# Kernel optimization log

Hardware: AMD Instinct MI355X
Metric: run time of the kernel (lower is better)

The kernel has to match this reference:

```python
import jax, jax.numpy as jnp
import numpy as np

H = 32        # num attention heads
KVH = 8       # num key/value heads
G = H // KVH  # kv groups
D = 128       # head dim
LATENT = 256
ROPE_BASE = 10000.0
LN_EPS = 1e-5


def setup_inputs() -> dict:
    key = jax.random.key(0)
    ks = jax.random.split(key, 8)
    B, S, H2 = 2, 1024, 8192
    s = 0.02  # weight init scale
    return {
        "hidden_states": jax.random.normal(ks[0], (B, S, H2), jnp.float32),
        "position_ids": jnp.sort(jax.random.randint(ks[1], (B, S), 0, S), axis=-1),
        "Wq": jax.random.normal(ks[2], (H * D, H2), jnp.float32) * s,
        "Wdkv": jax.random.normal(ks[3], (LATENT, H2), jnp.float32) * s,
        "ln_gamma": jnp.ones((LATENT,), jnp.float32),
        "ln_beta": jnp.zeros((LATENT,), jnp.float32),
        "Wuk": jax.random.normal(ks[4], (KVH * D, LATENT), jnp.float32) * s,
        "Wuv": jax.random.normal(ks[5], (KVH * D, LATENT), jnp.float32) * s,
        "Wo": jax.random.normal(ks[6], (H * D, H * D), jnp.float32) * s,
    }


def _rope_tables(seq_len, dim, dtype):
    inv_freq = 1.0 / (ROPE_BASE ** (jnp.arange(0, dim, 2, dtype=jnp.float32) / dim))
    t = jnp.arange(seq_len, dtype=jnp.float32)
    freqs = t[:, None] * inv_freq[None, :]          # [S, dim/2]
    emb = jnp.concatenate([freqs, freqs], axis=-1)  # [S, dim]
    return jnp.cos(emb).astype(dtype), jnp.sin(emb).astype(dtype)


def _rotate_half(x):
    x1, x2 = jnp.split(x, 2, axis=-1)
    return jnp.concatenate([-x2, x1], axis=-1)


def _apply_rope(x, cos, sin, position_ids):
    # x: [B, h, S, D]; cos/sin: [S_cache, D]; position_ids: [B, S]
    c = cos[position_ids][:, None]  # [B, 1, S, D]
    s = sin[position_ids][:, None]
    return x * c + _rotate_half(x) * s


def _layer_norm(x, gamma, beta):
    mu = jnp.mean(x, axis=-1, keepdims=True)
    var = jnp.mean(jnp.square(x - mu), axis=-1, keepdims=True)
    return (x - mu) * jax.lax.rsqrt(var + LN_EPS) * gamma + beta


def reference(hidden_states, position_ids, Wq, Wdkv, ln_gamma, ln_beta, Wuk, Wuv, Wo):
    B, S, _ = hidden_states.shape
    dtype = hidden_states.dtype

    # Q projection -> [B, H, S, D]
    q = (hidden_states @ Wq.T).reshape(B, S, H, D).transpose(0, 2, 1, 3)

    # MLA compress + norm: [B, S, LATENT]
    c_kv = _layer_norm(hidden_states @ Wdkv.T, ln_gamma, ln_beta)

    # RoPE on full head_dim (rope_dim == 0 path)
    cos, sin = _rope_tables(S, D, dtype)
    q = _apply_rope(q, cos, sin, position_ids)

    # Decompress K/V -> [B, KVH, S, D]
    k = (c_kv @ Wuk.T).reshape(B, S, KVH, D).transpose(0, 2, 1, 3)
    v = (c_kv @ Wuv.T).reshape(B, S, KVH, D).transpose(0, 2, 1, 3)
    k = _apply_rope(k, cos, sin, position_ids)

    # Grouped-query attention (repeat_kv expressed via group axis), causal
    qg = q.reshape(B, KVH, G, S, D)
    scale = 1.0 / jnp.sqrt(jnp.asarray(D, dtype))
    scores = jnp.einsum('bhgqd,bhkd->bhgqk', qg, k) * scale  # [B,KVH,G,S,S]
    causal = jnp.arange(S)[:, None] >= jnp.arange(S)[None, :]
    scores = jnp.where(causal, scores, jnp.asarray(-jnp.inf, dtype))
    probs = jax.nn.softmax(scores, axis=-1)
    attn = jnp.einsum('bhgqk,bhkd->bhgqd', probs, v)          # [B,KVH,G,S,D]
    attn = attn.reshape(B, H, S, D).transpose(0, 2, 1, 3).reshape(B, S, H * D)

    return attn @ Wo.T  # [B, S, hidden_size]
```

## Files before the change

### kernel.cpp

```cpp
#include <hip/hip_runtime.h>
#include <hip/hip_bf16.h>

using f32x4 = __attribute__((ext_vector_type(4))) float;
using s16x8 = __attribute__((ext_vector_type(8))) short;

__device__ __forceinline__ ushort f2b(float f) {
  union { float f; unsigned u; } v; v.f = f;
  unsigned r = v.u + 0x7fff + ((v.u >> 16) & 1);
  return (ushort)(r >> 16);
}
__device__ __forceinline__ float b2f(ushort u) {
  union { unsigned u; float f; } v; v.u = ((unsigned)u) << 16;
  return v.f;
}

__device__ __forceinline__ void load_lds16(const ushort* g, ushort* l) {
  __builtin_amdgcn_global_load_lds((const __attribute__((address_space(1))) unsigned int*)g,
                                   (__attribute__((address_space(3))) unsigned int*)l,
                                   16, 0, 0);
}

__device__ __forceinline__ void cast_seg(const float* __restrict__ in, ushort* __restrict__ out,
                                         int n8, int tid, int stride) {
  const float4* i4 = (const float4*)in;
  for (int i = tid; i < n8; i += stride) {
    float4 a = i4[i * 2];
    float4 b = i4[i * 2 + 1];
    s16x8 o;
    o[0] = f2b(a.x); o[1] = f2b(a.y); o[2] = f2b(a.z); o[3] = f2b(a.w);
    o[4] = f2b(b.x); o[5] = f2b(b.y); o[6] = f2b(b.z); o[7] = f2b(b.w);
    *(s16x8*)(out + (size_t)i * 8) = o;
  }
}

__global__ void cast6_kernel(const float* a0, ushort* b0, int n0,
                             const float* a1, ushort* b1, int n1,
                             const float* a2, ushort* b2, int n2,
                             const float* a3, ushort* b3, int n3,
                             const float* a4, ushort* b4, int n4,
                             const float* a5, ushort* b5, int n5) {
  int tid = blockIdx.x * blockDim.x + threadIdx.x;
  int stride = gridDim.x * blockDim.x;
  cast_seg(a0, b0, n0, tid, stride);
  cast_seg(a1, b1, n1, tid, stride);
  cast_seg(a2, b2, n2, tid, stride);
  cast_seg(a3, b3, n3, tid, stride);
  cast_seg(a4, b4, n4, tid, stride);
  cast_seg(a5, b5, n5, tid, stride);
}

__global__ void rope_table_kernel(const int* __restrict__ pos,
                                  float* __restrict__ cosb, float* __restrict__ sinb) {
  int i = blockIdx.x * 256 + threadIdx.x;
  int d = i & 63;
  float invf = exp2f(-(float)d * (13.287712379549449f / 64.0f));
  float ang = (float)pos[i >> 6] * invf;
  cosb[i] = cosf(ang);
  sinb[i] = sinf(ang);
}

__global__ void ln_kernel(const float* __restrict__ X, const float* __restrict__ gamma,
                          const float* __restrict__ beta, ushort* __restrict__ out) {
  int row = blockIdx.x * 4 + (threadIdx.x >> 6);
  int lane = threadIdx.x & 63;
  float4 x = {0.f, 0.f, 0.f, 0.f};
#pragma unroll
  for (int sp = 0; sp < 8; ++sp) {
    const float4 t = *(const float4*)(X + (size_t)sp * 2048 * 256 + (size_t)row * 256 + lane * 4);
    x.x += t.x; x.y += t.y; x.z += t.z; x.w += t.w;
  }
  float s = x.x + x.y + x.z + x.w;
  for (int m = 32; m >= 1; m >>= 1) s += __shfl_xor(s, m);
  float mu = s * (1.0f / 256.0f);
  float dx = x.x - mu, dy = x.y - mu, dz = x.z - mu, dw = x.w - mu;
  float v = dx * dx + dy * dy + dz * dz + dw * dw;
  for (int m = 32; m >= 1; m >>= 1) v += __shfl_xor(v, m);
  float inv = rsqrtf(v * (1.0f / 256.0f) + 1e-5f);
  const float4 g = *(const float4*)(gamma + lane * 4);
  const float4 bt = *(const float4*)(beta + lane * 4);
  ushort4 o;
  o.x = f2b(dx * inv * g.x + bt.x);
  o.y = f2b(dy * inv * g.y + bt.y);
  o.z = f2b(dz * inv * g.z + bt.z);
  o.w = f2b(dw * inv * g.w + bt.w);
  *(ushort4*)(out + (size_t)row * 256 + lane * 4) = o;
}

template<int NH>
__global__ void rope_apply_bf16(ushort* __restrict__ X, const float* __restrict__ cosb,
                                const float* __restrict__ sinb) {
  int bs = blockIdx.x;
  ushort* xr = X + (size_t)bs * (NH * 128);
  int p = threadIdx.x;
  if (p < NH * 8) {
    int h = p >> 3, c8 = p & 7;
    int idx = h * 128 + c8 * 8;
    s16x8 x1 = *(s16x8*)(xr + idx);
    s16x8 x2 = *(s16x8*)(xr + idx + 64);
    const float* cb = cosb + (bs << 6) + c8 * 8;
    const float* sb = sinb + (bs << 6) + c8 * 8;
    s16x8 o1, o2;
#pragma unroll
    for (int j = 0; j < 8; ++j) {
      float a = b2f((ushort)x1[j]), bb = b2f((ushort)x2[j]);
      float c = cb[j], s = sb[j];
      o1[j] = f2b(a * c - bb * s);
      o2[j] = f2b(bb * c + a * s);
    }
    *(s16x8*)(xr + idx) = o1;
    *(s16x8*)(xr + idx + 64) = o2;
  }
}

__global__ void qred_rope_kernel(const float* __restrict__ P, const float* __restrict__ cosb,
                                 const float* __restrict__ sinb, ushort* __restrict__ out) {
  int bs = blockIdx.x;
  int p = threadIdx.x;
  int h = p >> 3, c8 = p & 7;
  size_t base = (size_t)bs * 4096 + h * 128 + c8 * 8;
  const float* p0 = P + base;
  const float* p1 = P + 2048ull * 4096 + base;
  float4 a0 = *(const float4*)(p0);
  float4 a1 = *(const float4*)(p0 + 4);
  float4 b0 = *(const float4*)(p1);
  float4 b1 = *(const float4*)(p1 + 4);
  float4 c0 = *(const float4*)(p0 + 64);
  float4 c1 = *(const float4*)(p0 + 68);
  float4 d0 = *(const float4*)(p1 + 64);
  float4 d1 = *(const float4*)(p1 + 68);
  float x1[8] = {a0.x + b0.x, a0.y + b0.y, a0.z + b0.z, a0.w + b0.w,
                 a1.x + b1.x, a1.y + b1.y, a1.z + b1.z, a1.w + b1.w};
  float x2[8] = {c0.x + d0.x, c0.y + d0.y, c0.z + d0.z, c0.w + d0.w,
                 c1.x + d1.x, c1.y + d1.y, c1.z + d1.z, c1.w + d1.w};
  const float* cb = cosb + (bs << 6) + c8 * 8;
  const float* sb = sinb + (bs << 6) + c8 * 8;
  s16x8 o1, o2;
#pragma unroll
  for (int j = 0; j < 8; ++j) {
    float c = cb[j], s = sb[j];
    o1[j] = f2b(x1[j] * c - x2[j] * s);
    o2[j] = f2b(x2[j] * c + x1[j] * s);
  }
  ushort* orow = out + base;
  *(s16x8*)(orow) = o1;
  *(s16x8*)(orow + 64) = o2;
}

__global__ void ored_kernel(const float* __restrict__ P, float* __restrict__ out, int n4) {
  int stride = gridDim.x * blockDim.x;
  const float4* q0 = (const float4*)P;
  const float4* q1 = (const float4*)(P + 2048ull * 4096);
  for (int i = blockIdx.x * blockDim.x + threadIdx.x; i < n4; i += stride) {
    float4 a = q0[i], b = q1[i];
    float4 o = {a.x + b.x, a.y + b.y, a.z + b.z, a.w + b.w};
    ((float4*)out)[i] = o;
  }
}

__global__ __launch_bounds__(256, 2)
void gemm2_bt(const ushort* __restrict__ A, int lda, const ushort* __restrict__ B, int ldb,
              float* __restrict__ C, int M, int N, int Kloop) {
  __shared__ ushort lA[3][128 * 32];
  __shared__ ushort lB[3][256 * 32];
  const int gx = gridDim.x;
  const int nwg = gx * gridDim.y;
  const int bid = blockIdx.y * gx + blockIdx.x;
  const int cpx = nwg >> 3;
  const int swz = (bid & 7) * cpx + (bid >> 3);
  const int bm = (swz / gx) * 128;
  const int bn = (swz % gx) * 256;
  const int lane = threadIdx.x & 63;
  const int w = threadIdx.x >> 6;
  const int wm = w >> 1, wn = w & 1;
  const int l15 = lane & 15, l4 = lane >> 4;
  const int lr = lane >> 2;
  const int lc = lane & 3;

  f32x4 acc[4][8] = {};

  const ushort* Abase = A + (size_t)blockIdx.z * Kloop;
  const ushort* Bbase = B + (size_t)blockIdx.z * Kloop;

  auto stage = [&](int bb, int k0) {
#pragma unroll
    for (int p = 0; p < 2; ++p) {
      int row0 = w * 32 + p * 16;
      int r = row0 + lr;
      const ushort* src = Abase + (size_t)(bm + r) * lda + k0 + (lc ^ (r & 3)) * 8;
      load_lds16(src, &lA[bb][row0 * 32]);
    }
#pragma unroll
    for (int p = 0; p < 4; ++p) {
      int row0 = w * 64 + p * 16;
      int r = row0 + lr;
      const ushort* src = Bbase + (size_t)(bn + r) * ldb + k0 + (lc ^ (r & 3)) * 8;
      load_lds16(src, &lB[bb][row0 * 32]);
    }
  };

  const int nt = Kloop / 32;
  stage(0, 0);
  stage(1, 32);
  asm volatile("s_waitcnt vmcnt(6)" ::: "memory");
  __builtin_amdgcn_s_barrier();

  int cur = 0;
  for (int t = 0; t < nt; ++t) {
    if (t + 2 < nt) stage(cur == 0 ? 2 : cur - 1, (t + 2) * 32);
    __builtin_amdgcn_sched_barrier(0);
    s16x8 bf[8], af[4];
#pragma unroll
    for (int g = 0; g < 8; ++g) {
      int r = wn * 128 + g * 16 + l15;
      bf[g] = *(const s16x8*)&lB[cur][r * 32 + (l4 ^ (r & 3)) * 8];
    }
#pragma unroll
    for (int f = 0; f < 4; ++f) {
      int r = wm * 64 + f * 16 + l15;
      af[f] = *(const s16x8*)&lA[cur][r * 32 + (l4 ^ (r & 3)) * 8];
    }
    __builtin_amdgcn_s_setprio(1);
#pragma unroll
    for (int f = 0; f < 4; ++f)
#pragma unroll
      for (int g = 0; g < 8; ++g)
        acc[f][g] = __builtin_amdgcn_mfma_f32_16x16x32_bf16(af[f], bf[g], acc[f][g], 0, 0, 0);
    __builtin_amdgcn_s_setprio(0);
    __builtin_amdgcn_sched_barrier(0);
    if (t + 1 < nt) {
      if (t + 2 < nt) asm volatile("s_waitcnt vmcnt(6)" ::: "memory");
      else            asm volatile("s_waitcnt vmcnt(0)" ::: "memory");
      __builtin_amdgcn_s_barrier();
    }
    cur = (cur == 2) ? 0 : cur + 1;
  }

  const size_t cz = (size_t)blockIdx.z * M * N;
#pragma unroll
  for (int f = 0; f < 4; ++f)
#pragma unroll
    for (int g = 0; g < 8; ++g)
#pragma unroll
      for (int rr = 0; rr < 4; ++rr) {
        int row = bm + wm * 64 + f * 16 + l4 * 4 + rr;
        int col = bn + wn * 128 + g * 16 + l15;
        C[cz + (size_t)row * N + col] = acc[f][g][rr];
      }
}

template<bool BF16_OUT>
__global__ __launch_bounds__(256, 2)
void gemm_bt(const ushort* __restrict__ A, int lda, const ushort* __restrict__ B, int ldb,
             void* __restrict__ Cv, int M, int N, int Kloop) {
  __shared__ ushort lA[128 * 64];
  __shared__ ushort lB[128 * 64];
  const int nwg = gridDim.x * gridDim.y;
  const int bid = blockIdx.y * gridDim.x + blockIdx.x;
  const int cpx = nwg >> 3;
  const int swz = (bid & 7) * cpx + (bid >> 3);
  const int bm = (swz / gridDim.x) * 128;
  const int bn = (swz % gridDim.x) * 128;
  const int t = threadIdx.x;
  const int lane = t & 63;
  const int w = t >> 6;
  const int wr = (w >> 1) * 64, wc = (w & 1) * 64;
  const int l15 = lane & 15, l4 = lane >> 4;

  f32x4 acc[4][4] = {};

  const ushort* Ag = A + (size_t)blockIdx.z * Kloop +
                     (size_t)(bm + w * 8 + (lane >> 3)) * lda + (lane & 7) * 8;
  const ushort* Bg = B + (size_t)blockIdx.z * Kloop +
                     (size_t)(bn + w * 8 + (lane >> 3)) * ldb + (lane & 7) * 8;
  ushort* lAw = lA + w * 8 * 64;
  ushort* lBw = lB + w * 8 * 64;

  for (int k0 = 0; k0 < Kloop; k0 += 64) {
    __syncthreads();
#pragma unroll
    for (int p = 0; p < 4; ++p) {
      load_lds16(Ag + (size_t)(p * 32) * lda + k0, lAw + p * 32 * 64);
      load_lds16(Bg + (size_t)(p * 32) * ldb + k0, lBw + p * 32 * 64);
    }
    __syncthreads();
#pragma unroll
    for (int kk = 0; kk < 2; ++kk) {
      s16x8 af[4], bf[4];
#pragma unroll
      for (int i = 0; i < 4; ++i)
        af[i] = *(const s16x8*)(lA + (wr + i * 16 + l15) * 64 + kk * 32 + l4 * 8);
#pragma unroll
      for (int j = 0; j < 4; ++j)
        bf[j] = *(const s16x8*)(lB + (wc + j * 16 + l15) * 64 + kk * 32 + l4 * 8);
#pragma unroll
      for (int i = 0; i < 4; ++i)
#pragma unroll
        for (int j = 0; j < 4; ++j)
          acc[i][j] = __builtin_amdgcn_mfma_f32_16x16x32_bf16(af[i], bf[j], acc[i][j], 0, 0, 0);
    }
  }

  const size_t cz = (size_t)blockIdx.z * M * N;
#pragma unroll
  for (int i = 0; i < 4; ++i)
#pragma unroll
    for (int j = 0; j < 4; ++j)
#pragma unroll
      for (int r = 0; r < 4; ++r) {
        int row = bm + wr + i * 16 + l4 * 4 + r;
        int col = bn + wc + j * 16 + l15;
        if (BF16_OUT)
          ((ushort*)Cv)[cz + (size_t)row * N + col] = f2b(acc[i][j][r]);
        else
          ((float*)Cv)[cz + (size_t)row * N + col] = acc[i][j][r];
      }
}

__global__ __launch_bounds__(256, 2)
void attn_kernel(const ushort* __restrict__ Q, const ushort* __restrict__ Kb,
                 const ushort* __restrict__ Vt, ushort* __restrict__ O) {
  __shared__ ushort Kl[2][64 * 128];
  __shared__ ushort Vl[2][128 * 64];
  __shared__ ushort Plds[4][16][64];
  const int bx = blockIdx.x;
  const int qb = bx & 15;
  const int h = (bx >> 4) & 31;
  const int b = bx >> 9;
  const int kvh = h >> 2;
  const int w = threadIdx.x >> 6;
  const int lane = threadIdx.x & 63;
  const int l15 = lane & 15, l4 = lane >> 4;

  const int q0 = qb * 64 + w * 16;

  s16x8 aq[4];
  const ushort* qrow = Q + (size_t)(b * 1024 + q0 + l15) * 4096 + h * 128 + l4 * 8;
#pragma unroll
  for (int kk = 0; kk < 4; ++kk) aq[kk] = *(const s16x8*)(qrow + kk * 32);

  auto stageK = [&](int bb, int t) {
#pragma unroll
    for (int i = 0; i < 4; ++i) {
      int row = w * 16 + i * 4 + (lane >> 4);
      int cg = (lane & 15) ^ (row & 7);
      const ushort* src = Kb + (size_t)(b * 1024 + t * 64 + row) * 1024 + kvh * 128 + cg * 8;
      load_lds16(src, &Kl[bb][(w * 16 + i * 4) * 128]);
    }
  };
  auto stageV = [&](int bb, int t) {
#pragma unroll
    for (int i = 0; i < 4; ++i) {
      int d = w * 32 + i * 8 + (lane >> 3);
      int cg = (lane & 7) ^ (d & 7);
      const ushort* src = Vt + (size_t)(kvh * 128 + d) * 2048 + b * 1024 + t * 64 + cg * 8;
      load_lds16(src, &Vl[bb][(w * 32 + i * 8) * 64]);
    }
  };

  f32x4 o_acc[8] = {};
  float M_[4] = {-1e30f, -1e30f, -1e30f, -1e30f};
  float L_[4] = {0.f, 0.f, 0.f, 0.f};

  const int nt = qb + 1;
  int buf = 0;
  stageK(0, 0);
  stageV(0, 0);
  __syncthreads();

  for (int t = 0; t < nt; ++t) {
    if (t + 1 < nt) {
      stageK(buf ^ 1, t + 1);
      stageV(buf ^ 1, t + 1);
    }

    f32x4 s_acc[4] = {};
#pragma unroll
    for (int ns = 0; ns < 4; ++ns) {
      int r = ns * 16 + l15;
#pragma unroll
      for (int kk = 0; kk < 4; ++kk) {
        s16x8 kf = *(const s16x8*)&Kl[buf][r * 128 + (((kk * 4 + l4) ^ (r & 7)) * 8)];
        s_acc[ns] = __builtin_amdgcn_mfma_f32_16x16x32_bf16(aq[kk], kf, s_acc[ns], 0, 0, 0);
      }
    }

    float p[4][4];
    const bool diag = (t == qb);
#pragma unroll
    for (int ns = 0; ns < 4; ++ns)
#pragma unroll
      for (int r = 0; r < 4; ++r) {
        float s = s_acc[ns][r] * 0.08838834764831845f;
        if (diag) {
          int kvi = t * 64 + ns * 16 + l15;
          int qi = q0 + l4 * 4 + r;
          if (kvi > qi) s = -1e30f;
        }
        p[ns][r] = s;
      }

#pragma unroll
    for (int r = 0; r < 4; ++r) {
      float mt = fmaxf(fmaxf(p[0][r], p[1][r]), fmaxf(p[2][r], p[3][r]));
      mt = fmaxf(mt, __shfl_xor(mt, 1));
      mt = fmaxf(mt, __shfl_xor(mt, 2));
      mt = fmaxf(mt, __shfl_xor(mt, 4));
      mt = fmaxf(mt, __shfl_xor(mt, 8));
      float nm = fmaxf(M_[r], mt);
      float sf = __expf(M_[r] - nm);
      M_[r] = nm;
      float ls = 0.f;
#pragma unroll
      for (int ns = 0; ns < 4; ++ns) {
        float e = __expf(p[ns][r] - nm);
        p[ns][r] = e;
        ls += e;
      }
      ls += __shfl_xor(ls, 1);
      ls += __shfl_xor(ls, 2);
      ls += __shfl_xor(ls, 4);
      ls += __shfl_xor(ls, 8);
      L_[r] = L_[r] * sf + ls;
#pragma unroll
      for (int ds_ = 0; ds_ < 8; ++ds_) o_acc[ds_][r] *= sf;
    }

#pragma unroll
    for (int ns = 0; ns < 4; ++ns)
#pragma unroll
      for (int r = 0; r < 4; ++r)
        Plds[w][l4 * 4 + r][ns * 16 + l15] = f2b(p[ns][r]);
    asm volatile("s_waitcnt lgkmcnt(0)" ::: "memory");
    __builtin_amdgcn_sched_barrier(0);
    s16x8 pf[2];
    pf[0] = *(const s16x8*)&Plds[w][l15][l4 * 8];
    pf[1] = *(const s16x8*)&Plds[w][l15][32 + l4 * 8];

#pragma unroll
    for (int ds_ = 0; ds_ < 8; ++ds_) {
      int d = ds_ * 16 + l15;
#pragma unroll
      for (int kk2 = 0; kk2 < 2; ++kk2) {
        s16x8 vf = *(const s16x8*)&Vl[buf][d * 64 + (((kk2 * 4 + l4) ^ (d & 7)) * 8)];
        o_acc[ds_] = __builtin_amdgcn_mfma_f32_16x16x32_bf16(pf[kk2], vf, o_acc[ds_], 0, 0, 0);
      }
    }

    __syncthreads();
    buf ^= 1;
  }

#pragma unroll
  for (int r = 0; r < 4; ++r) {
    float invl = 1.0f / L_[r];
#pragma unroll
    for (int ds_ = 0; ds_ < 8; ++ds_)
      O[(size_t)(b * 1024 + q0 + l4 * 4 + r) * 4096 + h * 128 + ds_ * 16 + l15] =
          f2b(o_acc[ds_][r] * invl);
  }
}

extern "C" void kernel_launch(void* const* d_in, const int* in_sizes, int n_in,
                              void* d_out, int out_size, void* d_ws, size_t ws_size,
                              hipStream_t stream) {
  const float* hs = (const float*)d_in[0];
  const int* pos = (const int*)d_in[1];
  const float* Wq = (const float*)d_in[2];
  const float* Wdkv = (const float*)d_in[3];
  const float* gam = (const float*)d_in[4];
  const float* bet = (const float*)d_in[5];
  const float* Wuk = (const float*)d_in[6];
  const float* Wuv = (const float*)d_in[7];
  const float* Wo = (const float*)d_in[8];
  float* out = (float*)d_out;

  char* ws = (char*)d_ws;
  size_t off = 0;
  auto alloc = [&](size_t bytes) {
    char* p = ws + off;
    off += (bytes + 255) & ~(size_t)255;
    return p;
  };
  ushort* hs_b = (ushort*)alloc(2048ull * 8192 * 2);
  ushort* Wq_b = (ushort*)alloc(4096ull * 8192 * 2);
  ushort* Wdkv_b = (ushort*)alloc(256ull * 8192 * 2);
  ushort* Wuk_b = (ushort*)alloc(1024ull * 256 * 2);
  ushort* Wuv_b = (ushort*)alloc(1024ull * 256 * 2);
  ushort* Wo_b = (ushort*)alloc(4096ull * 4096 * 2);
  float* cosb = (float*)alloc(2048ull * 64 * 4);
  float* sinb = (float*)alloc(2048ull * 64 * 4);
  float* ckv_part = (float*)alloc(8ull * 2048 * 256 * 4);
  ushort* ckv_b = (ushort*)alloc(2048ull * 256 * 2);
  float* qo_part = (float*)alloc(2ull * 2048 * 4096 * 4);
  ushort* q_b = (ushort*)alloc(2048ull * 4096 * 2);
  ushort* k_b = (ushort*)alloc(2048ull * 1024 * 2);
  ushort* vt_b = (ushort*)alloc(1024ull * 2048 * 2);
  ushort* at_b = (ushort*)alloc(2048ull * 4096 * 2);
  (void)ws_size; (void)in_sizes; (void)n_in; (void)out_size;

  cast6_kernel<<<2048, 256, 0, stream>>>(
      hs, hs_b, (int)(2048ull * 8192 / 8),
      Wq, Wq_b, (int)(4096ull * 8192 / 8),
      Wdkv, Wdkv_b, (int)(256ull * 8192 / 8),
      Wuk, Wuk_b, (int)(1024ull * 256 / 8),
      Wuv, Wuv_b, (int)(1024ull * 256 / 8),
      Wo, Wo_b, (int)(4096ull * 4096 / 8));

  rope_table_kernel<<<512, 256, 0, stream>>>(pos, cosb, sinb);

  gemm_bt<false><<<dim3(2, 16, 8), 256, 0, stream>>>(hs_b, 8192, Wdkv_b, 8192,
                                                     ckv_part, 2048, 256, 1024);
  ln_kernel<<<512, 256, 0, stream>>>(ckv_part, gam, bet, ckv_b);

  gemm2_bt<<<dim3(16, 16, 2), 256, 0, stream>>>(hs_b, 8192, Wq_b, 8192,
                                                qo_part, 2048, 4096, 4096);
  qred_rope_kernel<<<2048, 256, 0, stream>>>(qo_part, cosb, sinb, q_b);

  gemm_bt<true><<<dim3(8, 16), 256, 0, stream>>>(ckv_b, 256, Wuk_b, 256,
                                                 k_b, 2048, 1024, 256);
  rope_apply_bf16<8><<<2048, 256, 0, stream>>>(k_b, cosb, sinb);

  gemm_bt<true><<<dim3(16, 8), 256, 0, stream>>>(Wuv_b, 256, ckv_b, 256,
                                                 vt_b, 1024, 2048, 256);

  attn_kernel<<<1024, 256, 0, stream>>>(q_b, k_b, vt_b, at_b);

  gemm2_bt<<<dim3(16, 16, 2), 256, 0, stream>>>(at_b, 4096, Wo_b, 4096,
                                                qo_part, 2048, 4096, 2048);
  ored_kernel<<<2048, 256, 0, stream>>>(qo_part, out, (int)(2048ull * 4096 / 4));
}
```

Baseline: 509.9 us.

## Replace split-K GEMM with 256x256-tile 8-wave kernel using ping-pong LDS phases

Replaces the 128x256-tile, 4-wave, triple-buffered GEMM used for the Q and output projections with a 256x256-tile, 8-wave kernel. It uses a K-step of 64, double buffering, and a four-phase schedule that interleaves LDS fragment reads with MFMA bursts, separated by barriers and priority changes. The larger tile raises arithmetic intensity per byte loaded and halves the number of workgroups. The cost is 128KB of LDS per block, which likely limits occupancy to one block per CU. It also adds many barriers per iteration and waits for all loads (vmcnt(0)) at the end of each step, which weakens load prefetching.

New measurement: 530.9 us. 4.1% more time.

```diff
diff --git a/kernel.cpp b/kernel.cpp
--- a/kernel.cpp
+++ b/kernel.cpp
@@ -3,6 +3,8 @@
 
 using f32x4 = __attribute__((ext_vector_type(4))) float;
 using s16x8 = __attribute__((ext_vector_type(8))) short;
+
+#define MFMA __builtin_amdgcn_mfma_f32_16x16x32_bf16
 
 __device__ __forceinline__ ushort f2b(float f) {
   union { float f; unsigned u; } v; v.f = f;
@@ -157,93 +159,132 @@
   }
 }
 
-__global__ __launch_bounds__(256, 2)
-void gemm2_bt(const ushort* __restrict__ A, int lda, const ushort* __restrict__ B, int ldb,
+__global__ __launch_bounds__(512, 2)
+void gemm8_bt(const ushort* __restrict__ A, int lda, const ushort* __restrict__ B, int ldb,
               float* __restrict__ C, int M, int N, int Kloop) {
-  __shared__ ushort lA[3][128 * 32];
-  __shared__ ushort lB[3][256 * 32];
+  __shared__ ushort lA[2][256 * 64];
+  __shared__ ushort lB[2][256 * 64];
   const int gx = gridDim.x;
   const int nwg = gx * gridDim.y;
   const int bid = blockIdx.y * gx + blockIdx.x;
   const int cpx = nwg >> 3;
   const int swz = (bid & 7) * cpx + (bid >> 3);
-  const int bm = (swz / gx) * 128;
+  const int bm = (swz / gx) * 256;
   const int bn = (swz % gx) * 256;
-  const int lane = threadIdx.x & 63;
-  const int w = threadIdx.x >> 6;
-  const int wm = w >> 1, wn = w & 1;
+  const int tid = threadIdx.x;
+  const int lane = tid & 63;
+  const int w = tid >> 6;
+  const int wm = w >> 2, wn = w & 3;
   const int l15 = lane & 15, l4 = lane >> 4;
-  const int lr = lane >> 2;
-  const int lc = lane & 3;
-
-  f32x4 acc[4][8] = {};
+
+  f32x4 acc[8][4] = {};
 
   const ushort* Abase = A + (size_t)blockIdx.z * Kloop;
   const ushort* Bbase = B + (size_t)blockIdx.z * Kloop;
+  const int srow = tid >> 3;
+  const int sswz = (tid & 7) ^ (srow & 7);
 
   auto stage = [&](int bb, int k0) {
-#pragma unroll
-    for (int p = 0; p < 2; ++p) {
-      int row0 = w * 32 + p * 16;
-      int r = row0 + lr;
-      const ushort* src = Abase + (size_t)(bm + r) * lda + k0 + (lc ^ (r & 3)) * 8;
-      load_lds16(src, &lA[bb][row0 * 32]);
-    }
-#pragma unroll
-    for (int p = 0; p < 4; ++p) {
-      int row0 = w * 64 + p * 16;
-      int r = row0 + lr;
-      const ushort* src = Bbase + (size_t)(bn + r) * ldb + k0 + (lc ^ (r & 3)) * 8;
-      load_lds16(src, &lB[bb][row0 * 32]);
-    }
+    const int rl = w * 8;
+#pragma unroll
+    for (int h = 0; h < 2; ++h)
+#pragma unroll
+      for (int p = 0; p < 2; ++p) {
+        int row = h * 128 + p * 64 + srow;
+        load_lds16(Abase + (size_t)(bm + row) * lda + k0 + sswz * 8,
+                   &lA[bb][(h * 128 + p * 64 + rl) * 64]);
+        load_lds16(Bbase + (size_t)(bn + row) * ldb + k0 + sswz * 8,
+                   &lB[bb][(h * 128 + p * 64 + rl) * 64]);
+      }
   };
-
-  const int nt = Kloop / 32;
+  auto rdA = [&](int bb, int f, int kk) -> s16x8 {
+    int r = wm * 128 + f * 16 + l15;
+    return *(const s16x8*)&lA[bb][r * 64 + ((kk * 4 + l4) ^ (l15 & 7)) * 8];
+  };
+  auto rdB = [&](int bb, int g, int kk) -> s16x8 {
+    int r = wn * 64 + g * 16 + l15;
+    return *(const s16x8*)&lB[bb][r * 64 + ((kk * 4 + l4) ^ (l15 & 7)) * 8];
+  };
+
+  const int nt = Kloop / 64;
   stage(0, 0);
-  stage(1, 32);
-  asm volatile("s_waitcnt vmcnt(6)" ::: "memory");
+  asm volatile("s_waitcnt vmcnt(0)" ::: "memory");
   __builtin_amdgcn_s_barrier();
 
-  int cur = 0;
+  s16x8 a[8], b[8];
   for (int t = 0; t < nt; ++t) {
-    if (t + 2 < nt) stage(cur == 0 ? 2 : cur - 1, (t + 2) * 32);
+    const int cur = t & 1;
+    if (t + 1 < nt) stage(cur ^ 1, (t + 1) * 64);
     __builtin_amdgcn_sched_barrier(0);
-    s16x8 bf[8], af[4];
-#pragma unroll
-    for (int g = 0; g < 8; ++g) {
-      int r = wn * 128 + g * 16 + l15;
-      bf[g] = *(const s16x8*)&lB[cur][r * 32 + (l4 ^ (r & 3)) * 8];
-    }
-#pragma unroll
-    for (int f = 0; f < 4; ++f) {
-      int r = wm * 64 + f * 16 + l15;
-      af[f] = *(const s16x8*)&lA[cur][r * 32 + (l4 ^ (r & 3)) * 8];
-    }
+#pragma unroll
+    for (int f = 0; f < 4; ++f) { a[2 * f] = rdA(cur, f, 0); a[2 * f + 1] = rdA(cur, f, 1); }
+    b[0] = rdB(cur, 0, 0); b[1] = rdB(cur, 0, 1);
+    b[2] = rdB(cur, 1, 0); b[3] = rdB(cur, 1, 1);
+    __builtin_amdgcn_s_barrier();
+    asm volatile("s_waitcnt lgkmcnt(0)" ::: "memory");
+    __builtin_amdgcn_sched_barrier(0);
     __builtin_amdgcn_s_setprio(1);
 #pragma unroll
     for (int f = 0; f < 4; ++f)
 #pragma unroll
-      for (int g = 0; g < 8; ++g)
-        acc[f][g] = __builtin_amdgcn_mfma_f32_16x16x32_bf16(af[f], bf[g], acc[f][g], 0, 0, 0);
+      for (int g = 0; g < 2; ++g) {
+        acc[f][g] = MFMA(a[2 * f], b[g * 2], acc[f][g], 0, 0, 0);
+        acc[f][g] = MFMA(a[2 * f + 1], b[g * 2 + 1], acc[f][g], 0, 0, 0);
+      }
     __builtin_amdgcn_s_setprio(0);
+    __builtin_amdgcn_s_barrier();
+    b[4] = rdB(cur, 2, 0); b[5] = rdB(cur, 2, 1);
+    b[6] = rdB(cur, 3, 0); b[7] = rdB(cur, 3, 1);
+    __builtin_amdgcn_s_barrier();
+    asm volatile("s_waitcnt lgkmcnt(0)" ::: "memory");
     __builtin_amdgcn_sched_barrier(0);
-    if (t + 1 < nt) {
-      if (t + 2 < nt) asm volatile("s_waitcnt vmcnt(6)" ::: "memory");
-      else            asm volatile("s_waitcnt vmcnt(0)" ::: "memory");
-      __builtin_amdgcn_s_barrier();
-    }
-    cur = (cur == 2) ? 0 : cur + 1;
+    __builtin_amdgcn_s_setprio(1);
+#pragma unroll
+    for (int f = 0; f < 4; ++f)
+#pragma unroll
+      for (int g = 2; g < 4; ++g) {
+        acc[f][g] = MFMA(a[2 * f], b[g * 2], acc[f][g], 0, 0, 0);
+        acc[f][g] = MFMA(a[2 * f + 1], b[g * 2 + 1], acc[f][g], 0, 0, 0);
+      }
+    __builtin_amdgcn_s_setprio(0);
+    __builtin_amdgcn_s_barrier();
+#pragma unroll
+    for (int f = 0; f < 4; ++f) { a[2 * f] = rdA(cur, 4 + f, 0); a[2 * f + 1] = rdA(cur, 4 + f, 1); }
+    __builtin_amdgcn_s_barrier();
+    asm volatile("s_waitcnt lgkmcnt(0)" ::: "memory");
+    __builtin_amdgcn_sched_barrier(0);
+    __builtin_amdgcn_s_setprio(1);
+#pragma unroll
+    for (int f = 0; f < 4; ++f)
+#pragma unroll
+      for (int g = 2; g < 4; ++g) {
+        acc[4 + f][g] = MFMA(a[2 * f], b[g * 2], acc[4 + f][g], 0, 0, 0);
+        acc[4 + f][g] = MFMA(a[2 * f + 1], b[g * 2 + 1], acc[4 + f][g], 0, 0, 0);
+      }
+    __builtin_amdgcn_s_setprio(0);
+    __builtin_amdgcn_s_barrier();
+    __builtin_amdgcn_s_setprio(1);
+#pragma unroll
+    for (int f = 0; f < 4; ++f)
+#pragma unroll
+      for (int g = 0; g < 2; ++g) {
+        acc[4 + f][g] = MFMA(a[2 * f], b[g * 2], acc[4 + f][g], 0, 0, 0);
+        acc[4 + f][g] = MFMA(a[2 * f + 1], b[g * 2 + 1], acc[4 + f][g], 0, 0, 0);
+      }
+    __builtin_amdgcn_s_setprio(0);
+    if (t + 1 < nt) asm volatile("s_waitcnt vmcnt(0)" ::: "memory");
+    __builtin_amdgcn_s_barrier();
   }
 
   const size_t cz = (size_t)blockIdx.z * M * N;
 #pragma unroll
-  for (int f = 0; f < 4; ++f)
-#pragma unroll
-    for (int g = 0; g < 8; ++g)
+  for (int f = 0; f < 8; ++f)
+#pragma unroll
+    for (int g = 0; g < 4; ++g)
 #pragma unroll
       for (int rr = 0; rr < 4; ++rr) {
-        int row = bm + wm * 64 + f * 16 + l4 * 4 + rr;
-        int col = bn + wn * 128 + g * 16 + l15;
+        int row = bm + wm * 128 + f * 16 + l4 * 4 + rr;
+        int col = bn + wn * 64 + g * 16 + l15;
         C[cz + (size_t)row * N + col] = acc[f][g][rr];
       }
 }
@@ -296,7 +337,7 @@
       for (int i = 0; i < 4; ++i)
 #pragma unroll
         for (int j = 0; j < 4; ++j)
-          acc[i][j] = __builtin_amdgcn_mfma_f32_16x16x32_bf16(af[i], bf[j], acc[i][j], 0, 0, 0);
+          acc[i][j] = MFMA(af[i], bf[j], acc[i][j], 0, 0, 0);
     }
   }
 
@@ -380,7 +421,7 @@
 #pragma unroll
       for (int kk = 0; kk < 4; ++kk) {
         s16x8 kf = *(const s16x8*)&Kl[buf][r * 128 + (((kk * 4 + l4) ^ (r & 7)) * 8)];
-        s_acc[ns] = __builtin_amdgcn_mfma_f32_16x16x32_bf16(aq[kk], kf, s_acc[ns], 0, 0, 0);
+        s_acc[ns] = MFMA(aq[kk], kf, s_acc[ns], 0, 0, 0);
       }
     }
 
@@ -442,7 +483,7 @@
 #pragma unroll
       for (int kk2 = 0; kk2 < 2; ++kk2) {
         s16x8 vf = *(const s16x8*)&Vl[buf][d * 64 + (((kk2 * 4 + l4) ^ (d & 7)) * 8)];
-        o_acc[ds_] = __builtin_amdgcn_mfma_f32_16x16x32_bf16(pf[kk2], vf, o_acc[ds_], 0, 0, 0);
+        o_acc[ds_] = MFMA(pf[kk2], vf, o_acc[ds_], 0, 0, 0);
       }
     }
 
@@ -512,8 +553,8 @@
                                                      ckv_part, 2048, 256, 1024);
   ln_kernel<<<512, 256, 0, stream>>>(ckv_part, gam, bet, ckv_b);
 
-  gemm2_bt<<<dim3(16, 16, 2), 256, 0, stream>>>(hs_b, 8192, Wq_b, 8192,
-                                                qo_part, 2048, 4096, 4096);
+  gemm8_bt<<<dim3(16, 8, 2), 512, 0, stream>>>(hs_b, 8192, Wq_b, 8192,
+                                               qo_part, 2048, 4096, 4096);
   qred_rope_kernel<<<2048, 256, 0, stream>>>(qo_part, cosb, sinb, q_b);
 
   gemm_bt<true><<<dim3(8, 16), 256, 0, stream>>>(ckv_b, 256, Wuk_b, 256,
@@ -525,7 +566,7 @@
 
   attn_kernel<<<1024, 256, 0, stream>>>(q_b, k_b, vt_b, at_b);
 
-  gemm2_bt<<<dim3(16, 16, 2), 256, 0, stream>>>(at_b, 4096, Wo_b, 4096,
-                                                qo_part, 2048, 4096, 2048);
+  gemm8_bt<<<dim3(16, 8, 2), 512, 0, stream>>>(at_b, 4096, Wo_b, 4096,
+                                               qo_part, 2048, 4096, 2048);
   ored_kernel<<<2048, 256, 0, stream>>>(qo_part, out, (int)(2048ull * 4096 / 4));
 }
```

## Enlarge attention query tile to 128 rows and store Q split-K partials as bf16

Applied to the files above, without the earlier changes.

The attention kernel now runs 512 threads (8 waves) over 128-query tiles, so each staged K/V tile is reused by twice as many query rows and the number of blocks is halved. Batch 1 walks its query blocks in reverse, and the diagonal mask check becomes per-wave. The Q projection GEMM now writes its two split-K partials as bf16 instead of fp32, and the reduce+RoPE kernel reads bf16, halving that traffic. The cost is some extra rounding error in the Q partial sums, plus wasted masked work for waves whose queries sit below the diagonal K tiles.

Measured after the change: 467.4 us. 1.09x faster.

```diff
diff --git a/kernel.cpp b/kernel.cpp
--- a/kernel.cpp
+++ b/kernel.cpp
@@ -3,6 +3,8 @@
 
 using f32x4 = __attribute__((ext_vector_type(4))) float;
 using s16x8 = __attribute__((ext_vector_type(8))) short;
+
+#define MFMA __builtin_amdgcn_mfma_f32_16x16x32_bf16
 
 __device__ __forceinline__ ushort f2b(float f) {
   union { float f; unsigned u; } v; v.f = f;
@@ -112,34 +114,26 @@
   }
 }
 
-__global__ void qred_rope_kernel(const float* __restrict__ P, const float* __restrict__ cosb,
+__global__ void qred_rope_kernel(const ushort* __restrict__ P, const float* __restrict__ cosb,
                                  const float* __restrict__ sinb, ushort* __restrict__ out) {
   int bs = blockIdx.x;
   int p = threadIdx.x;
   int h = p >> 3, c8 = p & 7;
   size_t base = (size_t)bs * 4096 + h * 128 + c8 * 8;
-  const float* p0 = P + base;
-  const float* p1 = P + 2048ull * 4096 + base;
-  float4 a0 = *(const float4*)(p0);
-  float4 a1 = *(const float4*)(p0 + 4);
-  float4 b0 = *(const float4*)(p1);
-  float4 b1 = *(const float4*)(p1 + 4);
-  float4 c0 = *(const float4*)(p0 + 64);
-  float4 c1 = *(const float4*)(p0 + 68);
-  float4 d0 = *(const float4*)(p1 + 64);
-  float4 d1 = *(const float4*)(p1 + 68);
-  float x1[8] = {a0.x + b0.x, a0.y + b0.y, a0.z + b0.z, a0.w + b0.w,
-                 a1.x + b1.x, a1.y + b1.y, a1.z + b1.z, a1.w + b1.w};
-  float x2[8] = {c0.x + d0.x, c0.y + d0.y, c0.z + d0.z, c0.w + d0.w,
-                 c1.x + d1.x, c1.y + d1.y, c1.z + d1.z, c1.w + d1.w};
+  s16x8 a0 = *(const s16x8*)(P + base);
+  s16x8 b0 = *(const s16x8*)(P + 2048ull * 4096 + base);
+  s16x8 c0 = *(const s16x8*)(P + base + 64);
+  s16x8 d0 = *(const s16x8*)(P + 2048ull * 4096 + base + 64);
   const float* cb = cosb + (bs << 6) + c8 * 8;
   const float* sb = sinb + (bs << 6) + c8 * 8;
   s16x8 o1, o2;
 #pragma unroll
   for (int j = 0; j < 8; ++j) {
+    float x1 = b2f((ushort)a0[j]) + b2f((ushort)b0[j]);
+    float x2 = b2f((ushort)c0[j]) + b2f((ushort)d0[j]);
     float c = cb[j], s = sb[j];
-    o1[j] = f2b(x1[j] * c - x2[j] * s);
-    o2[j] = f2b(x2[j] * c + x1[j] * s);
+    o1[j] = f2b(x1 * c - x2 * s);
+    o2[j] = f2b(x2 * c + x1 * s);
   }
   ushort* orow = out + base;
   *(s16x8*)(orow) = o1;
@@ -157,9 +151,10 @@
   }
 }
 
+template<bool BF16_OUT>
 __global__ __launch_bounds__(256, 2)
 void gemm2_bt(const ushort* __restrict__ A, int lda, const ushort* __restrict__ B, int ldb,
-              float* __restrict__ C, int M, int N, int Kloop) {
+              void* __restrict__ Cv, int M, int N, int Kloop) {
   __shared__ ushort lA[3][128 * 32];
   __shared__ ushort lB[3][256 * 32];
   const int gx = gridDim.x;
@@ -224,7 +219,7 @@
     for (int f = 0; f < 4; ++f)
 #pragma unroll
       for (int g = 0; g < 8; ++g)
-        acc[f][g] = __builtin_amdgcn_mfma_f32_16x16x32_bf16(af[f], bf[g], acc[f][g], 0, 0, 0);
+        acc[f][g] = MFMA(af[f], bf[g], acc[f][g], 0, 0, 0);
     __builtin_amdgcn_s_setprio(0);
     __builtin_amdgcn_sched_barrier(0);
     if (t + 1 < nt) {
@@ -244,7 +239,10 @@
       for (int rr = 0; rr < 4; ++rr) {
         int row = bm + wm * 64 + f * 16 + l4 * 4 + rr;
         int col = bn + wn * 128 + g * 16 + l15;
-        C[cz + (size_t)row * N + col] = acc[f][g][rr];
+        if (BF16_OUT)
+          ((ushort*)Cv)[cz + (size_t)row * N + col] = f2b(acc[f][g][rr]);
+        else
+          ((float*)Cv)[cz + (size_t)row * N + col] = acc[f][g][rr];
       }
 }
 
@@ -296,7 +294,7 @@
       for (int i = 0; i < 4; ++i)
 #pragma unroll
         for (int j = 0; j < 4; ++j)
-          acc[i][j] = __builtin_amdgcn_mfma_f32_16x16x32_bf16(af[i], bf[j], acc[i][j], 0, 0, 0);
+          acc[i][j] = MFMA(af[i], bf[j], acc[i][j], 0, 0, 0);
     }
   }
 
@@ -316,22 +314,22 @@
       }
 }
 
-__global__ __launch_bounds__(256, 2)
+__global__ __launch_bounds__(512, 2)
 void attn_kernel(const ushort* __restrict__ Q, const ushort* __restrict__ Kb,
                  const ushort* __restrict__ Vt, ushort* __restrict__ O) {
   __shared__ ushort Kl[2][64 * 128];
   __shared__ ushort Vl[2][128 * 64];
-  __shared__ ushort Plds[4][16][64];
+  __shared__ ushort Plds[8][16][64];
   const int bx = blockIdx.x;
-  const int qb = bx & 15;
-  const int h = (bx >> 4) & 31;
-  const int b = bx >> 9;
+  const int b = bx >> 8;
+  const int qb = b ? (7 - (bx & 7)) : (bx & 7);
+  const int h = (bx >> 3) & 31;
   const int kvh = h >> 2;
   const int w = threadIdx.x >> 6;
   const int lane = threadIdx.x & 63;
   const int l15 = lane & 15, l4 = lane >> 4;
 
-  const int q0 = qb * 64 + w * 16;
+  const int q0 = qb * 128 + w * 16;
 
   s16x8 aq[4];
   const ushort* qrow = Q + (size_t)(b * 1024 + q0 + l15) * 4096 + h * 128 + l4 * 8;
@@ -340,20 +338,22 @@
 
   auto stageK = [&](int bb, int t) {
 #pragma unroll
-    for (int i = 0; i < 4; ++i) {
-      int row = w * 16 + i * 4 + (lane >> 4);
+    for (int i = 0; i < 2; ++i) {
+      int row0 = w * 8 + i * 4;
+      int row = row0 + (lane >> 4);
       int cg = (lane & 15) ^ (row & 7);
       const ushort* src = Kb + (size_t)(b * 1024 + t * 64 + row) * 1024 + kvh * 128 + cg * 8;
-      load_lds16(src, &Kl[bb][(w * 16 + i * 4) * 128]);
+      load_lds16(src, &Kl[bb][row0 * 128]);
     }
   };
   auto stageV = [&](int bb, int t) {
 #pragma unroll
-    for (int i = 0; i < 4; ++i) {
-      int d = w * 32 + i * 8 + (lane >> 3);
+    for (int i = 0; i < 2; ++i) {
+      int d0 = w * 16 + i * 8;
+      int d = d0 + (lane >> 3);
       int cg = (lane & 7) ^ (d & 7);
       const ushort* src = Vt + (size_t)(kvh * 128 + d) * 2048 + b * 1024 + t * 64 + cg * 8;
-      load_lds16(src, &Vl[bb][(w * 32 + i * 8) * 64]);
+      load_lds16(src, &Vl[bb][d0 * 64]);
     }
   };
 
@@ -361,7 +361,7 @@
   float M_[4] = {-1e30f, -1e30f, -1e30f, -1e30f};
   float L_[4] = {0.f, 0.f, 0.f, 0.f};
 
-  const int nt = qb + 1;
+  const int nt = 2 * qb + 2;
   int buf = 0;
   stageK(0, 0);
   stageV(0, 0);
@@ -380,12 +380,12 @@
 #pragma unroll
       for (int kk = 0; kk < 4; ++kk) {
         s16x8 kf = *(const s16x8*)&Kl[buf][r * 128 + (((kk * 4 + l4) ^ (r & 7)) * 8)];
-        s_acc[ns] = __builtin_amdgcn_mfma_f32_16x16x32_bf16(aq[kk], kf, s_acc[ns], 0, 0, 0);
+        s_acc[ns] = MFMA(aq[kk], kf, s_acc[ns], 0, 0, 0);
       }
     }
 
     float p[4][4];
-    const bool diag = (t == qb);
+    const bool diag = (t * 64 + 63 > q0);
 #pragma unroll
     for (int ns = 0; ns < 4; ++ns)
 #pragma unroll
@@ -442,7 +442,7 @@
 #pragma unroll
       for (int kk2 = 0; kk2 < 2; ++kk2) {
         s16x8 vf = *(const s16x8*)&Vl[buf][d * 64 + (((kk2 * 4 + l4) ^ (d & 7)) * 8)];
-        o_acc[ds_] = __builtin_amdgcn_mfma_f32_16x16x32_bf16(pf[kk2], vf, o_acc[ds_], 0, 0, 0);
+        o_acc[ds_] = MFMA(pf[kk2], vf, o_acc[ds_], 0, 0, 0);
       }
     }
 
@@ -492,6 +492,7 @@
   float* ckv_part = (float*)alloc(8ull * 2048 * 256 * 4);
   ushort* ckv_b = (ushort*)alloc(2048ull * 256 * 2);
   float* qo_part = (float*)alloc(2ull * 2048 * 4096 * 4);
+  ushort* qp_b = (ushort*)alloc(2ull * 2048 * 4096 * 2);
   ushort* q_b = (ushort*)alloc(2048ull * 4096 * 2);
   ushort* k_b = (ushort*)alloc(2048ull * 1024 * 2);
   ushort* vt_b = (ushort*)alloc(1024ull * 2048 * 2);
@@ -512,9 +513,9 @@
                                                      ckv_part, 2048, 256, 1024);
   ln_kernel<<<512, 256, 0, stream>>>(ckv_part, gam, bet, ckv_b);
 
-  gemm2_bt<<<dim3(16, 16, 2), 256, 0, stream>>>(hs_b, 8192, Wq_b, 8192,
-                                                qo_part, 2048, 4096, 4096);
-  qred_rope_kernel<<<2048, 256, 0, stream>>>(qo_part, cosb, sinb, q_b);
+  gemm2_bt<true><<<dim3(16, 16, 2), 256, 0, stream>>>(hs_b, 8192, Wq_b, 8192,
+                                                      qp_b, 2048, 4096, 4096);
+  qred_rope_kernel<<<2048, 256, 0, stream>>>(qp_b, cosb, sinb, q_b);
 
   gemm_bt<true><<<dim3(8, 16), 256, 0, stream>>>(ckv_b, 256, Wuk_b, 256,
                                                  k_b, 2048, 1024, 256);
@@ -523,9 +524,9 @@
   gemm_bt<true><<<dim3(16, 8), 256, 0, stream>>>(Wuv_b, 256, ckv_b, 256,
                                                  vt_b, 1024, 2048, 256);
 
-  attn_kernel<<<1024, 256, 0, stream>>>(q_b, k_b, vt_b, at_b);
-
-  gemm2_bt<<<dim3(16, 16, 2), 256, 0, stream>>>(at_b, 4096, Wo_b, 4096,
-                                                qo_part, 2048, 4096, 2048);
+  attn_kernel<<<512, 512, 0, stream>>>(q_b, k_b, vt_b, at_b);
+
+  gemm2_bt<false><<<dim3(16, 16, 2), 256, 0, stream>>>(at_b, 4096, Wo_b, 4096,
+                                                       qo_part, 2048, 4096, 2048);
   ored_kernel<<<2048, 256, 0, stream>>>(qo_part, out, (int)(2048ull * 4096 / 4));
 }
```
